# Performance work log

Hardware: AMD Instinct MI355X
Metric: run time of the kernel (lower is better)

The kernel has to match this reference:

```python
import jax, jax.numpy as jnp
import numpy as np

DIM = 256
KERNEL_DIM = 128
NUM_MASKS = 100


def setup_inputs() -> dict:
    key = jax.random.key(0)
    ks = jax.random.split(key, 12)
    B, C, H, W = 8, DIM, 128, 128
    features = jax.random.normal(ks[0], (B, C, H, W), dtype=jnp.float32)
    # iam conv: normal std=0.01 weights, bias = -log((1-p)/p), p=0.01
    bias_value = -np.log((1 - 0.01) / 0.01)
    conv_w = 0.01 * jax.random.normal(ks[1], (NUM_MASKS, C, 3, 3), dtype=jnp.float32)
    conv_b = jnp.full((NUM_MASKS,), bias_value, dtype=jnp.float32)
    # fc: xavier-uniform-like fill (c2_xavier_fill)
    limit = np.sqrt(6.0 / (C + C)).astype(np.float32)
    fc_w = jax.random.uniform(ks[2], (C, C), minval=-limit, maxval=limit, dtype=jnp.float32)
    fc_b = jnp.zeros((C,), dtype=jnp.float32)
    cls_w = 0.01 * jax.random.normal(ks[3], (1, C), dtype=jnp.float32)
    cls_b = jnp.full((1,), bias_value, dtype=jnp.float32)
    mk_w = 0.01 * jax.random.normal(ks[4], (KERNEL_DIM, C), dtype=jnp.float32)
    mk_b = jnp.zeros((KERNEL_DIM,), dtype=jnp.float32)
    obj_w = (1.0 / np.sqrt(C)) * jax.random.normal(ks[5], (1, C), dtype=jnp.float32)
    obj_b = jnp.zeros((1,), dtype=jnp.float32)
    softmax_bias = jnp.ones((1,), dtype=jnp.float32)
    return dict(features=features, conv_w=conv_w, conv_b=conv_b,
                softmax_bias=softmax_bias, fc_w=fc_w, fc_b=fc_b,
                cls_w=cls_w, cls_b=cls_b, mk_w=mk_w, mk_b=mk_b,
                obj_w=obj_w, obj_b=obj_b)


def reference(features, conv_w, conv_b, softmax_bias, fc_w, fc_b,
              cls_w, cls_b, mk_w, mk_b, obj_w, obj_b):
    B, C, H, W = features.shape
    N = conv_w.shape[0]
    # 3x3 conv, padding=1, groups=1 (num_groups == 1)
    iam = jax.lax.conv_general_dilated(
        features, conv_w, window_strides=(1, 1), padding=((1, 1), (1, 1)),
        dimension_numbers=('NCHW', 'OIHW', 'NCHW'))
    iam = iam + conv_b[None, :, None, None]          # (B, N, H, W)
    # softmax over flattened HW with learned scalar bias
    iam_flat = iam.reshape(B, N, H * W)
    iam_prob = jax.nn.softmax(iam_flat + softmax_bias, axis=-1)  # (B, N, HW)
    # attention-weighted spatial pooling of conv features
    feat_flat = features.reshape(B, C, H * W)
    inst = jnp.einsum('bnp,bcp->bnc', iam_prob, feat_flat)       # (B, N, C)
    # num_groups == 1: the reshape/transpose is identity
    inst = jax.nn.relu(inst @ fc_w.T + fc_b)
    pred_logits = inst @ cls_w.T + cls_b
    pred_kernel = inst @ mk_w.T + mk_b
    pred_scores = inst @ obj_w.T + obj_b
    return pred_logits, pred_kernel, pred_scores, iam
```

## Files before the change

### kernel.cpp

```cpp
#include <hip/hip_runtime.h>
#include <math.h>

#define BATCH 8
#define CHAN 256
#define HH 128
#define WW 128
#define NMASK 100
#define HWSZ (HH*WW)
#define KD 128

#define OFF_LOGITS 0
#define OFF_KERNEL 800
#define OFF_SCORES (800 + 800*KD)
#define OFF_IAM    (OFF_SCORES + 800)

typedef __attribute__((ext_vector_type(8))) short bf16x8;
typedef __attribute__((ext_vector_type(8))) unsigned short ushort8;
typedef __attribute__((ext_vector_type(4))) float f32x4;

#define WCHUNK (9*7*64*8)

__device__ __forceinline__ unsigned short f2bf(float f){
  unsigned int u = __float_as_uint(f);
  u += 0x7fffu + ((u >> 16) & 1u);
  return (unsigned short)(u >> 16);
}

__global__ __launch_bounds__(256) void wpack_kernel(
    const float* __restrict__ cw, unsigned short* __restrict__ wr,
    float* __restrict__ rowsum)
{
  if (blockIdx.x == 0){
    for (int i = threadIdx.x; i < BATCH*NMASK; i += 256) rowsum[i] = 0.f;
  }
  int i = blockIdx.x*256 + threadIdx.x;
  if (i >= 8*9*7*64*8) return;
  int j = i & 7;
  int l = (i >> 3) & 63;
  int rest = i >> 9;
  int nt = rest % 7;
  int tc = rest / 7;
  int tap = tc % 9;
  int cc  = tc / 9;
  int n = nt*16 + (l & 15);
  int c = cc*32 + (l >> 4)*8 + j;
  float v = 0.f;
  if (n < NMASK) v = cw[((size_t)n*CHAN + c)*9 + tap];
  wr[i] = f2bf(v);
}

__global__ __launch_bounds__(256) void prepack_feat_kernel(
    const float* __restrict__ feat, unsigned short* __restrict__ feath)
{
  const int b  = blockIdx.z;
  const int cg = blockIdx.y;
  const int t  = threadIdx.x;
  __shared__ unsigned short lt[8*264];
  const int cl = t >> 5;
  const int po = (t & 31)*8;
  for (int st=0; st<8; ++st){
    const int P0 = blockIdx.x*2048 + st*256;
    const float* src = feat + ((size_t)(b*CHAN + cg*8 + cl))*HWSZ + P0 + po;
    float4 a0 = *(const float4*)src;
    float4 a1 = *(const float4*)(src+4);
    ushort8 u;
    u[0]=f2bf(a0.x); u[1]=f2bf(a0.y); u[2]=f2bf(a0.z); u[3]=f2bf(a0.w);
    u[4]=f2bf(a1.x); u[5]=f2bf(a1.y); u[6]=f2bf(a1.z); u[7]=f2bf(a1.w);
    *(ushort8*)&lt[cl*264 + po] = u;
    __syncthreads();
    ushort8 v;
    #pragma unroll
    for (int c=0;c<8;c++) v[c] = lt[c*264 + t];
    *(ushort8*)&feath[(((size_t)b*32 + cg)*HWSZ + P0 + t)*8] = v;
    __syncthreads();
  }
}

__global__ __launch_bounds__(256,2) void conv_mfma4_kernel(
    const unsigned short* __restrict__ feath, const unsigned short* __restrict__ wr,
    const float* __restrict__ cb, float* __restrict__ out_iam)
{
  const int h0 = blockIdx.x*2;
  const int b  = blockIdx.y;
  const int t  = threadIdx.x;
  const int w  = t >> 6;
  const int l  = t & 63;
  const int lx = l & 15;
  const int lg = l >> 4;

  __shared__ unsigned short lA[WCHUNK];

  f32x4 acc[7][2][2];
  #pragma unroll
  for (int nt=0;nt<7;nt++)
    #pragma unroll
    for (int r=0;r<2;r++)
      #pragma unroll
      for (int pi=0;pi<2;pi++) acc[nt][r][pi] = (f32x4){0.f,0.f,0.f,0.f};

  const unsigned short* fb = feath + ((size_t)b*32 + lg)*HWSZ*8;
  const int xb0 = (w*2+0)*16 + lx - 1;
  const int xb1 = (w*2+1)*16 + lx - 1;

  #pragma unroll 1
  for (int cc=0; cc<8; ++cc){
    __syncthreads();
    {
      const unsigned short* src = wr + (size_t)cc*WCHUNK;
      #pragma unroll
      for (int it=0; it<16; ++it){
        int g2 = it*4 + w;
        if (g2 < 63){
          ushort8 v = *(const ushort8*)(src + ((size_t)g2*64 + l)*8);
          *(ushort8*)&lA[((size_t)g2*64 + l)*8] = v;
        }
      }
    }
    __syncthreads();

    const unsigned short* fcc = fb + (size_t)cc*4*HWSZ*8;
    #pragma unroll
    for (int tap=0; tap<9; ++tap){
      const int kh = tap/3, kw = tap - 3*(tap/3);
      bf16x8 a[7];
      #pragma unroll
      for (int nt=0;nt<7;nt++)
        a[nt] = *(const bf16x8*)&lA[(((size_t)tap*7+nt)*64 + l)*8];
      bf16x8 bv[2][2];
      #pragma unroll
      for (int r=0;r<2;r++){
        const int hr = h0 + r + kh - 1;
        const bool rvv = (unsigned)hr < 128u;
        const int hc = rvv ? hr : 0;
        #pragma unroll
        for (int pi=0;pi<2;pi++){
          const int X = (pi ? xb1 : xb0) + kw;
          const bool xv = (unsigned)X < 128u;
          const int Xc = xv ? X : 0;
          bf16x8 v2 = *(const bf16x8*)&fcc[((size_t)hc*WW + Xc)*8];
          bv[r][pi] = (rvv && xv) ? v2 : (bf16x8)(short)0;
        }
      }
      #pragma unroll
      for (int nt=0;nt<7;nt++)
        #pragma unroll
        for (int r=0;r<2;r++)
          #pragma unroll
          for (int pi=0;pi<2;pi++)
            acc[nt][r][pi] = __builtin_amdgcn_mfma_f32_16x16x32_bf16(
                a[nt], bv[r][pi], acc[nt][r][pi], 0, 0, 0);
    }
  }

  #pragma unroll
  for (int nt=0; nt<7; nt++){
    const int n0 = nt*16 + lg*4;
    #pragma unroll
    for (int r=0; r<2; r++){
      #pragma unroll
      for (int pi=0; pi<2; pi++){
        const int xo = (w*2+pi)*16 + lx;
        #pragma unroll
        for (int q=0; q<4; q++){
          int n = n0 + q;
          if (n < NMASK)
            out_iam[((size_t)b*NMASK + n)*HWSZ + (h0+r)*WW + xo] = acc[nt][r][pi][q] + cb[n];
        }
      }
    }
  }
}

#define LDSX 40
__global__ __launch_bounds__(256) void conv_mfma_kernel(
    const float* __restrict__ feat, const unsigned short* __restrict__ wr,
    const float* __restrict__ cb, float* __restrict__ out_iam)
{
  const int h = blockIdx.x;
  const int b = blockIdx.y;
  const int t = threadIdx.x;
  const int w = t >> 6;
  const int l = t & 63;
  const int lx = l & 15;
  const int lg = l >> 4;

  __shared__ unsigned short lds[3*132*LDSX];

  f32x4 acc[7][2];
  #pragma unroll
  for (int nt=0;nt<7;nt++)
    #pragma unroll
    for (int pi=0;pi<2;pi++) acc[nt][pi] = (f32x4){0.f,0.f,0.f,0.f};

  const float* fb = feat + (size_t)b*CHAN*HWSZ;

  for (int cc=0; cc<8; ++cc){
    const int c0 = cc*32;
    __syncthreads();
    for (int gi = t; gi < 1560; gi += 256){
      int xh = gi % 130;
      int q  = gi / 130;
      int cg = q & 3;
      int kh = q >> 2;
      int row = h + kh - 1;
      int xx  = xh - 1;
      bool ok = ((unsigned)row < 128u) & ((unsigned)xx < 128u);
      const float* src = fb + (size_t)(c0 + cg*8)*HWSZ + row*WW + xx;
      ushort8 u;
      #pragma unroll
      for (int j=0;j<8;j++){
        float v = ok ? src[(size_t)j*HWSZ] : 0.f;
        u[j] = f2bf(v);
      }
      *(ushort8*)&lds[(kh*132 + xh)*LDSX + cg*8] = u;
    }
    __syncthreads();

    const unsigned short* wbase = wr + ((size_t)cc*9*7*64 + l)*8;
    #pragma unroll 1
    for (int tap=0; tap<9; ++tap){
      const int kh = tap / 3;
      const int kw = tap - kh*3;
      bf16x8 a[7];
      #pragma unroll
      for (int nt=0; nt<7; nt++)
        a[nt] = *(const bf16x8*)(wbase + ((size_t)(tap*7 + nt))*64*8);
      bf16x8 bfv[2];
      #pragma unroll
      for (int pi=0; pi<2; pi++){
        int xh = (w*2+pi)*16 + lx + kw;
        bfv[pi] = *(const bf16x8*)&lds[(kh*132 + xh)*LDSX + lg*8];
      }
      #pragma unroll
      for (int nt=0; nt<7; nt++)
        #pragma unroll
        for (int pi=0; pi<2; pi++)
          acc[nt][pi] = __builtin_amdgcn_mfma_f32_16x16x32_bf16(
              a[nt], bfv[pi], acc[nt][pi], 0, 0, 0);
    }
  }

  #pragma unroll
  for (int nt=0; nt<7; nt++){
    const int n0 = nt*16 + lg*4;
    #pragma unroll
    for (int pi=0; pi<2; pi++){
      const int xo = (w*2+pi)*16 + lx;
      #pragma unroll
      for (int r=0; r<4; r++){
        int n = n0 + r;
        if (n < NMASK)
          out_iam[((size_t)b*NMASK + n)*HWSZ + h*WW + xo] = acc[nt][pi][r] + cb[n];
      }
    }
  }
}

__global__ __launch_bounds__(256) void einsum_mfma_kernel(
  const float* __restrict__ feat, const float* __restrict__ iam,
  float* __restrict__ rowsum, float* __restrict__ partial)
{
  const int s = blockIdx.x;
  const int nsplit = gridDim.x;
  const int KC = HWSZ / nsplit;
  const int b = blockIdx.z;
  const int t = threadIdx.x;
  const int w = t >> 6;
  const int l = t & 63;
  const int lx = l & 15;
  const int lg = l >> 4;

  f32x4 acc[7][4];
  #pragma unroll
  for (int nt=0;nt<7;nt++)
    #pragma unroll
    for (int j=0;j<4;j++) acc[nt][j] = (f32x4){0.f,0.f,0.f,0.f};

  float se[7];
  #pragma unroll
  for (int nt=0;nt<7;nt++) se[nt] = 0.f;

  int rown[7];
  #pragma unroll
  for (int nt=0;nt<7;nt++){
    int row = nt*16 + lx;
    if (row >= NMASK) row = NMASK-1;
    rown[nt] = row;
  }

  const float* fb = feat + (size_t)b*CHAN*HWSZ;
  const float* ib = iam  + (size_t)b*NMASK*HWSZ;

  #pragma unroll 1
  for (int ks=0; ks<KC/32; ++ks){
    const int p0 = s*KC + ks*32 + lg*8;
    bf16x8 afr[7];
    #pragma unroll
    for (int nt=0;nt<7;nt++){
      const float* ap = ib + (size_t)rown[nt]*HWSZ + p0;
      float4 a0 = *(const float4*)ap;
      float4 a1 = *(const float4*)(ap+4);
      float e0=__expf(a0.x), e1=__expf(a0.y), e2=__expf(a0.z), e3=__expf(a0.w);
      float e4=__expf(a1.x), e5=__expf(a1.y), e6=__expf(a1.z), e7=__expf(a1.w);
      se[nt] += (e0+e1)+(e2+e3)+((e4+e5)+(e6+e7));
      ushort8 u;
      u[0]=f2bf(e0); u[1]=f2bf(e1); u[2]=f2bf(e2); u[3]=f2bf(e3);
      u[4]=f2bf(e4); u[5]=f2bf(e5); u[6]=f2bf(e6); u[7]=f2bf(e7);
      afr[nt] = *(bf16x8*)&u;
    }
    bf16x8 bfr[4];
    #pragma unroll
    for (int j=0;j<4;j++){
      const float* fp = fb + (size_t)(w*64 + j*16 + lx)*HWSZ + p0;
      float4 b0 = *(const float4*)fp;
      float4 b1 = *(const float4*)(fp+4);
      ushort8 u;
      u[0]=f2bf(b0.x); u[1]=f2bf(b0.y); u[2]=f2bf(b0.z); u[3]=f2bf(b0.w);
      u[4]=f2bf(b1.x); u[5]=f2bf(b1.y); u[6]=f2bf(b1.z); u[7]=f2bf(b1.w);
      bfr[j] = *(bf16x8*)&u;
    }
    #pragma unroll
    for (int nt=0;nt<7;nt++)
      #pragma unroll
      for (int j=0;j<4;j++)
        acc[nt][j] = __builtin_amdgcn_mfma_f32_16x16x32_bf16(
            afr[nt], bfr[j], acc[nt][j], 0, 0, 0);
  }

  if (w == 0){
    #pragma unroll
    for (int nt=0;nt<7;nt++){
      float sv = se[nt];
      sv += __shfl_xor(sv, 16);
      sv += __shfl_xor(sv, 32);
      int row = nt*16 + l;
      if (l < 16 && row < NMASK)
        atomicAdd(&rowsum[b*NMASK + row], sv);
    }
  }

  #pragma unroll
  for (int nt=0;nt<7;nt++){
    #pragma unroll
    for (int j=0;j<4;j++){
      const int c = w*64 + j*16 + lx;
      #pragma unroll
      for (int r=0;r<4;r++){
        int n = nt*16 + lg*4 + r;
        if (n < NMASK)
          partial[(((size_t)b*nsplit + s)*NMASK + n)*CHAN + c] = acc[nt][j][r];
      }
    }
  }
}

__global__ __launch_bounds__(256) void fc_head_kernel(
  const float* __restrict__ partial, int nsplit,
  const float* __restrict__ rowsum,
  const float* __restrict__ fc_w, const float* __restrict__ fc_b,
  const float* __restrict__ cls_w, const float* __restrict__ cls_b,
  const float* __restrict__ mk_w, const float* __restrict__ mk_b,
  const float* __restrict__ obj_w, const float* __restrict__ obj_b,
  float* __restrict__ dout)
{
  const int n = blockIdx.x;
  const int b = blockIdx.y;
  const int t = threadIdx.x;
  __shared__ float xs[256];
  __shared__ float xr[256];
  __shared__ float red[256];
  float x = 0.f;
  for (int s=0;s<nsplit;s++)
    x += partial[(((size_t)b*nsplit+s)*NMASK + n)*CHAN + t];
  x *= (1.0f / rowsum[b*NMASK + n]);
  xs[t] = x;
  __syncthreads();
  float y = fc_b[t];
  const float* wr2 = fc_w + (size_t)t*CHAN;
  for (int k=0;k<CHAN;k+=4){
    float4 w4 = *(const float4*)&wr2[k];
    y = fmaf(xs[k],w4.x,y); y=fmaf(xs[k+1],w4.y,y);
    y = fmaf(xs[k+2],w4.z,y); y=fmaf(xs[k+3],w4.w,y);
  }
  y = fmaxf(y, 0.f);
  xr[t] = y;
  __syncthreads();
  if (t < KD){
    float ka = mk_b[t];
    const float* mr = mk_w + (size_t)t*CHAN;
    for (int k=0;k<CHAN;k+=4){
      float4 w4 = *(const float4*)&mr[k];
      ka = fmaf(xr[k],w4.x,ka); ka=fmaf(xr[k+1],w4.y,ka);
      ka = fmaf(xr[k+2],w4.z,ka); ka=fmaf(xr[k+3],w4.w,ka);
    }
    dout[OFF_KERNEL + ((size_t)b*NMASK + n)*KD + t] = ka;
  }
  red[t] = xr[t] * cls_w[t];
  __syncthreads();
  for (int s2=128;s2>0;s2>>=1){ if(t<s2) red[t]+=red[t+s2]; __syncthreads(); }
  if (t==0) dout[OFF_LOGITS + (size_t)b*NMASK + n] = red[0] + cls_b[0];
  __syncthreads();
  red[t] = xr[t] * obj_w[t];
  __syncthreads();
  for (int s2=128;s2>0;s2>>=1){ if(t<s2) red[t]+=red[t+s2]; __syncthreads(); }
  if (t==0) dout[OFF_SCORES + (size_t)b*NMASK + n] = red[0] + obj_b[0];
}

extern "C" void kernel_launch(void* const* d_in, const int* in_sizes, int n_in,
                              void* d_out, int out_size, void* d_ws, size_t ws_size,
                              hipStream_t stream)
{
  const float* feat   = (const float*)d_in[0];
  const float* conv_w = (const float*)d_in[1];
  const float* conv_b = (const float*)d_in[2];
  const float* fc_w   = (const float*)d_in[4];
  const float* fc_b   = (const float*)d_in[5];
  const float* cls_w  = (const float*)d_in[6];
  const float* cls_b  = (const float*)d_in[7];
  const float* mk_w   = (const float*)d_in[8];
  const float* mk_b   = (const float*)d_in[9];
  const float* obj_w  = (const float*)d_in[10];
  const float* obj_b  = (const float*)d_in[11];
  float* dout = (float*)d_out;
  float* iam  = dout + OFF_IAM;

  const size_t statb  = 1600*sizeof(float);
  const size_t wrb    = (size_t)8*WCHUNK*2;
  const size_t feathb = (size_t)BATCH*32*HWSZ*8*2;

  float* rowsum  = (float*)d_ws;
  unsigned short* wr = (unsigned short*)((char*)d_ws + statb);
  char* shared_region = (char*)d_ws + statb + wrb;

  wpack_kernel<<<dim3((8*WCHUNK + 255)/256), 256, 0, stream>>>(conv_w, wr, rowsum);

  if (ws_size >= statb + wrb + feathb + 1024){
    unsigned short* feath = (unsigned short*)shared_region;
    float* partial = (float*)shared_region;
    const int ksplit = 64;
    prepack_feat_kernel<<<dim3(8,32,8), 256, 0, stream>>>(feat, feath);
    conv_mfma4_kernel<<<dim3(64, 8), 256, 0, stream>>>(feath, wr, conv_b, iam);
    einsum_mfma_kernel<<<dim3(ksplit, 1, 8), 256, 0, stream>>>(feat, iam, rowsum, partial);
    fc_head_kernel<<<dim3(NMASK,BATCH), 256, 0, stream>>>(partial, ksplit, rowsum,
        fc_w, fc_b, cls_w, cls_b, mk_w, mk_b, obj_w, obj_b, dout);
  } else {
    float* partial = (float*)shared_region;
    int ksplit = 16;
    if (ws_size >= statb + wrb + (size_t)32*BATCH*NMASK*CHAN*4) ksplit = 32;
    conv_mfma_kernel<<<dim3(128, 8), 256, 0, stream>>>(feat, wr, conv_b, iam);
    einsum_mfma_kernel<<<dim3(ksplit, 1, 8), 256, 0, stream>>>(feat, iam, rowsum, partial);
    fc_head_kernel<<<dim3(NMASK,BATCH), 256, 0, stream>>>(partial, ksplit, rowsum,
        fc_w, fc_b, cls_w, cls_b, mk_w, mk_b, obj_w, obj_b, dout);
  }
}
```

Measured before the change: 221.7 us.

## Emit bf16 exp(iam) from conv epilogue and consume it in einsum

The conv epilogue now also computes exp of each iam value and stores it as bf16 in a new workspace buffer. A new einsum kernel reads these precomputed bf16 exponentials directly as MFMA A operands instead of reading fp32 iam and exponentiating it. This moves the exp work into the conv and halves the bytes the einsum reads for the attention map. The cost is an extra 26MB write in the conv, a larger workspace requirement for the fast path, and exp taken without max subtraction, which relies on the logits being small.

```diff
diff --git a/kernel.cpp b/kernel.cpp
--- a/kernel.cpp
+++ b/kernel.cpp
@@ -76,9 +76,10 @@
   }
 }
 
-__global__ __launch_bounds__(256,2) void conv_mfma4_kernel(
+__global__ __launch_bounds__(256,2) void conv_mfma4e_kernel(
     const unsigned short* __restrict__ feath, const unsigned short* __restrict__ wr,
-    const float* __restrict__ cb, float* __restrict__ out_iam)
+    const float* __restrict__ cb, float* __restrict__ out_iam,
+    unsigned short* __restrict__ expi)
 {
   const int h0 = blockIdx.x*2;
   const int b  = blockIdx.y;
@@ -163,8 +164,12 @@
         #pragma unroll
         for (int q=0; q<4; q++){
           int n = n0 + q;
-          if (n < NMASK)
-            out_iam[((size_t)b*NMASK + n)*HWSZ + (h0+r)*WW + xo] = acc[nt][r][pi][q] + cb[n];
+          if (n < NMASK){
+            const float v = acc[nt][r][pi][q] + cb[n];
+            const size_t idx = ((size_t)b*NMASK + n)*HWSZ + (h0+r)*WW + xo;
+            out_iam[idx] = v;
+            expi[idx] = f2bf(__expf(v));
+          }
         }
       }
     }
@@ -251,6 +256,99 @@
         int n = n0 + r;
         if (n < NMASK)
           out_iam[((size_t)b*NMASK + n)*HWSZ + h*WW + xo] = acc[nt][pi][r] + cb[n];
+      }
+    }
+  }
+}
+
+__global__ __launch_bounds__(256) void einsum_expi_kernel(
+  const float* __restrict__ feat, const unsigned short* __restrict__ expi,
+  float* __restrict__ rowsum, float* __restrict__ partial)
+{
+  const int s = blockIdx.x;
+  const int nsplit = gridDim.x;
+  const int KC = HWSZ / nsplit;
+  const int b = blockIdx.z;
+  const int t = threadIdx.x;
+  const int w = t >> 6;
+  const int l = t & 63;
+  const int lx = l & 15;
+  const int lg = l >> 4;
+
+  f32x4 acc[7][4];
+  #pragma unroll
+  for (int nt=0;nt<7;nt++)
+    #pragma unroll
+    for (int j=0;j<4;j++) acc[nt][j] = (f32x4){0.f,0.f,0.f,0.f};
+
+  float se[7];
+  #pragma unroll
+  for (int nt=0;nt<7;nt++) se[nt] = 0.f;
+
+  int rown[7];
+  #pragma unroll
+  for (int nt=0;nt<7;nt++){
+    int row = nt*16 + lx;
+    if (row >= NMASK) row = NMASK-1;
+    rown[nt] = row;
+  }
+
+  const float* fb = feat + (size_t)b*CHAN*HWSZ;
+  const unsigned short* eb = expi + (size_t)b*NMASK*HWSZ;
+
+  #pragma unroll 1
+  for (int ks=0; ks<KC/32; ++ks){
+    const int p0 = s*KC + ks*32 + lg*8;
+    bf16x8 afr[7];
+    #pragma unroll
+    for (int nt=0;nt<7;nt++){
+      ushort8 u = *(const ushort8*)(eb + (size_t)rown[nt]*HWSZ + p0);
+      #pragma unroll
+      for (int j=0;j<8;j++)
+        se[nt] += __uint_as_float((unsigned)u[j] << 16);
+      afr[nt] = *(bf16x8*)&u;
+    }
+    bf16x8 bfr[4];
+    #pragma unroll
+    for (int j=0;j<4;j++){
+      const float* fp = fb + (size_t)(w*64 + j*16 + lx)*HWSZ + p0;
+      float4 b0 = *(const float4*)fp;
+      float4 b1 = *(const float4*)(fp+4);
+      ushort8 u;
+      u[0]=f2bf(b0.x); u[1]=f2bf(b0.y); u[2]=f2bf(b0.z); u[3]=f2bf(b0.w);
+      u[4]=f2bf(b1.x); u[5]=f2bf(b1.y); u[6]=f2bf(b1.z); u[7]=f2bf(b1.w);
+      bfr[j] = *(bf16x8*)&u;
+    }
+    #pragma unroll
+    for (int nt=0;nt<7;nt++)
+      #pragma unroll
+      for (int j=0;j<4;j++)
+        acc[nt][j] = __builtin_amdgcn_mfma_f32_16x16x32_bf16(
+            afr[nt], bfr[j], acc[nt][j], 0, 0, 0);
+  }
+
+  if (w == 0){
+    #pragma unroll
+    for (int nt=0;nt<7;nt++){
+      float sv = se[nt];
+      sv += __shfl_xor(sv, 16);
+      sv += __shfl_xor(sv, 32);
+      int row = nt*16 + l;
+      if (l < 16 && row < NMASK)
+        atomicAdd(&rowsum[b*NMASK + row], sv);
+    }
+  }
+
+  #pragma unroll
+  for (int nt=0;nt<7;nt++){
+    #pragma unroll
+    for (int j=0;j<4;j++){
+      const int c = w*64 + j*16 + lx;
+      #pragma unroll
+      for (int r=0;r<4;r++){
+        int n = nt*16 + lg*4 + r;
+        if (n < NMASK)
+          partial[(((size_t)b*nsplit + s)*NMASK + n)*CHAN + c] = acc[nt][j][r];
       }
     }
   }
@@ -427,20 +525,22 @@
   const size_t statb  = 1600*sizeof(float);
   const size_t wrb    = (size_t)8*WCHUNK*2;
   const size_t feathb = (size_t)BATCH*32*HWSZ*8*2;
-
-  float* rowsum  = (float*)d_ws;
+  const size_t expib  = (size_t)BATCH*NMASK*HWSZ*2;
+
+  float* rowsum = (float*)d_ws;
   unsigned short* wr = (unsigned short*)((char*)d_ws + statb);
   char* shared_region = (char*)d_ws + statb + wrb;
+  unsigned short* expi = (unsigned short*)(shared_region + feathb);
 
   wpack_kernel<<<dim3((8*WCHUNK + 255)/256), 256, 0, stream>>>(conv_w, wr, rowsum);
 
-  if (ws_size >= statb + wrb + feathb + 1024){
+  if (ws_size >= statb + wrb + feathb + expib + 1024){
     unsigned short* feath = (unsigned short*)shared_region;
     float* partial = (float*)shared_region;
     const int ksplit = 64;
     prepack_feat_kernel<<<dim3(8,32,8), 256, 0, stream>>>(feat, feath);
-    conv_mfma4_kernel<<<dim3(64, 8), 256, 0, stream>>>(feath, wr, conv_b, iam);
-    einsum_mfma_kernel<<<dim3(ksplit, 1, 8), 256, 0, stream>>>(feat, iam, rowsum, partial);
+    conv_mfma4e_kernel<<<dim3(64, 8), 256, 0, stream>>>(feath, wr, conv_b, iam, expi);
+    einsum_expi_kernel<<<dim3(ksplit, 1, 8), 256, 0, stream>>>(feat, expi, rowsum, partial);
     fc_head_kernel<<<dim3(NMASK,BATCH), 256, 0, stream>>>(partial, ksplit, rowsum,
         fc_w, fc_b, cls_w, cls_b, mk_w, mk_b, obj_w, obj_b, dout);
   } else {
```

Measured after the change: 217.8 us. No clear change (-1.7%).

## Fuse exp into conv epilogue and store bf16 exp map and partials

Applied to the files above, without the earlier changes.

The conv epilogue now also computes exp of the logits and writes it as a bf16 buffer. The einsum kernel reads this half-size buffer instead of re-reading the fp32 iam and recomputing exp, and it builds the row sums from the bf16 values. The split-K partials are stored as bf16 to halve that traffic, and the einsum loop is unrolled by 2. This adds an extra bf16 write in the conv kernel and lowers precision for the row sums and partial accumulation. The fallback path's workspace requirement changes without any size check.

```diff
diff --git a/kernel.cpp b/kernel.cpp
--- a/kernel.cpp
+++ b/kernel.cpp
@@ -76,9 +76,10 @@
   }
 }
 
-__global__ __launch_bounds__(256,2) void conv_mfma4_kernel(
+__global__ __launch_bounds__(256,2) void conv_mfma4e_kernel(
     const unsigned short* __restrict__ feath, const unsigned short* __restrict__ wr,
-    const float* __restrict__ cb, float* __restrict__ out_iam)
+    const float* __restrict__ cb, float* __restrict__ out_iam,
+    unsigned short* __restrict__ expi)
 {
   const int h0 = blockIdx.x*2;
   const int b  = blockIdx.y;
@@ -163,8 +164,12 @@
         #pragma unroll
         for (int q=0; q<4; q++){
           int n = n0 + q;
-          if (n < NMASK)
-            out_iam[((size_t)b*NMASK + n)*HWSZ + (h0+r)*WW + xo] = acc[nt][r][pi][q] + cb[n];
+          if (n < NMASK){
+            const float v = acc[nt][r][pi][q] + cb[n];
+            const size_t idx = ((size_t)b*NMASK + n)*HWSZ + (h0+r)*WW + xo;
+            out_iam[idx] = v;
+            expi[idx] = f2bf(__expf(v));
+          }
         }
       }
     }
@@ -174,7 +179,8 @@
 #define LDSX 40
 __global__ __launch_bounds__(256) void conv_mfma_kernel(
     const float* __restrict__ feat, const unsigned short* __restrict__ wr,
-    const float* __restrict__ cb, float* __restrict__ out_iam)
+    const float* __restrict__ cb, float* __restrict__ out_iam,
+    unsigned short* __restrict__ expi)
 {
   const int h = blockIdx.x;
   const int b = blockIdx.y;
@@ -249,16 +255,20 @@
       #pragma unroll
       for (int r=0; r<4; r++){
         int n = n0 + r;
-        if (n < NMASK)
-          out_iam[((size_t)b*NMASK + n)*HWSZ + h*WW + xo] = acc[nt][pi][r] + cb[n];
-      }
-    }
-  }
-}
-
-__global__ __launch_bounds__(256) void einsum_mfma_kernel(
-  const float* __restrict__ feat, const float* __restrict__ iam,
-  float* __restrict__ rowsum, float* __restrict__ partial)
+        if (n < NMASK){
+          const float v = acc[nt][pi][r] + cb[n];
+          const size_t idx = ((size_t)b*NMASK + n)*HWSZ + h*WW + xo;
+          out_iam[idx] = v;
+          expi[idx] = f2bf(__expf(v));
+        }
+      }
+    }
+  }
+}
+
+__global__ __launch_bounds__(256) void einsum_expi_kernel(
+  const float* __restrict__ feat, const unsigned short* __restrict__ expi,
+  float* __restrict__ rowsum, unsigned short* __restrict__ partial)
 {
   const int s = blockIdx.x;
   const int nsplit = gridDim.x;
@@ -289,23 +299,18 @@
   }
 
   const float* fb = feat + (size_t)b*CHAN*HWSZ;
-  const float* ib = iam  + (size_t)b*NMASK*HWSZ;
-
-  #pragma unroll 1
+  const unsigned short* eb = expi + (size_t)b*NMASK*HWSZ;
+
+  #pragma unroll 2
   for (int ks=0; ks<KC/32; ++ks){
     const int p0 = s*KC + ks*32 + lg*8;
     bf16x8 afr[7];
     #pragma unroll
     for (int nt=0;nt<7;nt++){
-      const float* ap = ib + (size_t)rown[nt]*HWSZ + p0;
-      float4 a0 = *(const float4*)ap;
-      float4 a1 = *(const float4*)(ap+4);
-      float e0=__expf(a0.x), e1=__expf(a0.y), e2=__expf(a0.z), e3=__expf(a0.w);
-      float e4=__expf(a1.x), e5=__expf(a1.y), e6=__expf(a1.z), e7=__expf(a1.w);
-      se[nt] += (e0+e1)+(e2+e3)+((e4+e5)+(e6+e7));
-      ushort8 u;
-      u[0]=f2bf(e0); u[1]=f2bf(e1); u[2]=f2bf(e2); u[3]=f2bf(e3);
-      u[4]=f2bf(e4); u[5]=f2bf(e5); u[6]=f2bf(e6); u[7]=f2bf(e7);
+      ushort8 u = *(const ushort8*)(eb + (size_t)rown[nt]*HWSZ + p0);
+      #pragma unroll
+      for (int j=0;j<8;j++)
+        se[nt] += __uint_as_float((unsigned)u[j] << 16);
       afr[nt] = *(bf16x8*)&u;
     }
     bf16x8 bfr[4];
@@ -348,14 +353,14 @@
       for (int r=0;r<4;r++){
         int n = nt*16 + lg*4 + r;
         if (n < NMASK)
-          partial[(((size_t)b*nsplit + s)*NMASK + n)*CHAN + c] = acc[nt][j][r];
+          partial[(((size_t)b*nsplit + s)*NMASK + n)*CHAN + c] = f2bf(acc[nt][j][r]);
       }
     }
   }
 }
 
 __global__ __launch_bounds__(256) void fc_head_kernel(
-  const float* __restrict__ partial, int nsplit,
+  const unsigned short* __restrict__ partial, int nsplit,
   const float* __restrict__ rowsum,
   const float* __restrict__ fc_w, const float* __restrict__ fc_b,
   const float* __restrict__ cls_w, const float* __restrict__ cls_b,
@@ -371,7 +376,7 @@
   __shared__ float red[256];
   float x = 0.f;
   for (int s=0;s<nsplit;s++)
-    x += partial[(((size_t)b*nsplit+s)*NMASK + n)*CHAN + t];
+    x += __uint_as_float((unsigned)partial[(((size_t)b*nsplit+s)*NMASK + n)*CHAN + t] << 16);
   x *= (1.0f / rowsum[b*NMASK + n]);
   xs[t] = x;
   __syncthreads();
@@ -427,28 +432,30 @@
   const size_t statb  = 1600*sizeof(float);
   const size_t wrb    = (size_t)8*WCHUNK*2;
   const size_t feathb = (size_t)BATCH*32*HWSZ*8*2;
-
-  float* rowsum  = (float*)d_ws;
+  const size_t expib  = (size_t)BATCH*NMASK*HWSZ*2;
+
+  float* rowsum = (float*)d_ws;
   unsigned short* wr = (unsigned short*)((char*)d_ws + statb);
   char* shared_region = (char*)d_ws + statb + wrb;
+  unsigned short* expi = (unsigned short*)(shared_region + feathb);
 
   wpack_kernel<<<dim3((8*WCHUNK + 255)/256), 256, 0, stream>>>(conv_w, wr, rowsum);
 
-  if (ws_size >= statb + wrb + feathb + 1024){
+  if (ws_size >= statb + wrb + feathb + expib + 1024){
     unsigned short* feath = (unsigned short*)shared_region;
-    float* partial = (float*)shared_region;
+    unsigned short* partial = (unsigned short*)shared_region;
     const int ksplit = 64;
     prepack_feat_kernel<<<dim3(8,32,8), 256, 0, stream>>>(feat, feath);
-    conv_mfma4_kernel<<<dim3(64, 8), 256, 0, stream>>>(feath, wr, conv_b, iam);
-    einsum_mfma_kernel<<<dim3(ksplit, 1, 8), 256, 0, stream>>>(feat, iam, rowsum, partial);
+    conv_mfma4e_kernel<<<dim3(64, 8), 256, 0, stream>>>(feath, wr, conv_b, iam, expi);
+    einsum_expi_kernel<<<dim3(ksplit, 1, 8), 256, 0, stream>>>(feat, expi, rowsum, partial);
     fc_head_kernel<<<dim3(NMASK,BATCH), 256, 0, stream>>>(partial, ksplit, rowsum,
         fc_w, fc_b, cls_w, cls_b, mk_w, mk_b, obj_w, obj_b, dout);
   } else {
-    float* partial = (float*)shared_region;
-    int ksplit = 16;
-    if (ws_size >= statb + wrb + (size_t)32*BATCH*NMASK*CHAN*4) ksplit = 32;
-    conv_mfma_kernel<<<dim3(128, 8), 256, 0, stream>>>(feat, wr, conv_b, iam);
-    einsum_mfma_kernel<<<dim3(ksplit, 1, 8), 256, 0, stream>>>(feat, iam, rowsum, partial);
+    unsigned short* expiB = (unsigned short*)shared_region;
+    unsigned short* partial = (unsigned short*)(shared_region + expib);
+    int ksplit = 32;
+    conv_mfma_kernel<<<dim3(128, 8), 256, 0, stream>>>(feat, wr, conv_b, iam, expiB);
+    einsum_expi_kernel<<<dim3(ksplit, 1, 8), 256, 0, stream>>>(feat, expiB, rowsum, partial);
     fc_head_kernel<<<dim3(NMASK,BATCH), 256, 0, stream>>>(partial, ksplit, rowsum,
         fc_w, fc_b, cls_w, cls_b, mk_w, mk_b, obj_w, obj_b, dout);
   }
```

Result: faster. 215.6 us (-2.7%).
